# Optimization experiments

Measured on AMD Instinct MI355X. Metric: run time of the kernel, lower is better.

The kernel has to match this reference:

```python
import math
import jax, jax.numpy as jnp
import numpy as np

N_IMAGES = 32
TOTAL_Q = 2048
TOTAL_KV = 2048
Q_IN = 1024
KV_IN = Q_IN + 9
D_QK = 1024
D_V = 1024
N_HEADS = 16
TEMP = 1.0
SCALER = 1.0 / (TEMP * math.sqrt(D_QK // N_HEADS))


def _ragged_seg_ids(total, n_seg, seed):
    rng = np.random.default_rng(seed)
    lens = rng.multinomial(total - n_seg, np.ones(n_seg) / n_seg) + 1  # every segment nonempty
    return jnp.asarray(np.repeat(np.arange(n_seg), lens), dtype=jnp.int32)


def setup_inputs() -> dict:
    key = jax.random.key(0)
    ks = jax.random.split(key, 12)
    s = 0.02
    return {
        "A": jax.random.normal(ks[0], (TOTAL_Q, Q_IN), jnp.float32),
        "B0": jax.random.normal(ks[1], (TOTAL_KV, KV_IN), jnp.float32),
        "seg_q": _ragged_seg_ids(TOTAL_Q, N_IMAGES, 1),
        "seg_kv": _ragged_seg_ids(TOTAL_KV, N_IMAGES, 2),
        "Wq": jax.random.normal(ks[2], (Q_IN, D_QK), jnp.float32) * s,
        "bq": jax.random.normal(ks[3], (D_QK,), jnp.float32) * s,
        "Wk": jax.random.normal(ks[4], (KV_IN, D_QK), jnp.float32) * s,
        "bk": jax.random.normal(ks[5], (D_QK,), jnp.float32) * s,
        "Wv": jax.random.normal(ks[6], (KV_IN, D_V), jnp.float32) * s,
        "bv": jax.random.normal(ks[7], (D_V,), jnp.float32) * s,
        "Wf": jax.random.normal(ks[8], (D_V, Q_IN), jnp.float32) * s,
        "bf": jax.random.normal(ks[9], (Q_IN,), jnp.float32) * s,
    }


def reference(A, B0, seg_q, seg_kv, Wq, bq, Wk, bk, Wv, bv, Wf, bf):
    # Linear projections on packed rows
    q = (A @ Wq + bq).reshape(TOTAL_Q, N_HEADS, -1)     # [Nq, h, dqk]
    k = (B0 @ Wk + bk).reshape(TOTAL_KV, N_HEADS, -1)   # [Nk, h, dqk]
    v = (B0 @ Wv + bv).reshape(TOTAL_KV, N_HEADS, -1)   # [Nk, h, dv]
    # Per-segment attention expressed as a block mask (same math as the
    # original Python loop over splits)
    scores = jnp.einsum('ihd,khd->ihk', q, k) * SCALER  # [Nq, h, Nk]
    mask = (seg_q[:, None] == seg_kv[None, :])[:, None, :]  # [Nq, 1, Nk]
    neg = jnp.finfo(scores.dtype).min
    w = jax.nn.softmax(jnp.where(mask, scores, neg), axis=-1)
    wv = jnp.einsum('ihk,khd->ihd', w, v).reshape(TOTAL_Q, -1)  # [Nq, h*dv]
    return wv @ Wf + bf  # [Nq, q_in_dim]
```

## Files before the change

### kernel.cpp

```cpp
#include <hip/hip_runtime.h>
#include <hip/hip_bf16.h>
#include <math.h>

#define TOTAL_Q   2048
#define TOTAL_KV  2048
#define QIN       1024
#define KVIN      1033
#define KVIN_P    1056
#define DQK       1024
#define DV        1024
#define KVSTR     2048
#define SCALER    0.125f

typedef __bf16 bf16x8 __attribute__((ext_vector_type(8)));
typedef float  f32x4  __attribute__((ext_vector_type(4)));

__device__ __forceinline__ void glds16(const __hip_bfloat16* g, __bf16* l)
{
    __builtin_amdgcn_global_load_lds(
        (const __attribute__((address_space(1))) void*)g,
        (__attribute__((address_space(3))) void*)l,
        16, 0, 0);
}

__global__ __launch_bounds__(256)
void prep_k(const float* __restrict__ A,  const float* __restrict__ B0,
            const float* __restrict__ Wq, const float* __restrict__ Wk,
            const float* __restrict__ Wv, const float* __restrict__ Wf,
            const float* __restrict__ bf,
            __hip_bfloat16* __restrict__ Abf, __hip_bfloat16* __restrict__ B0bf,
            __hip_bfloat16* __restrict__ Wqt, __hip_bfloat16* __restrict__ Wkt,
            __hip_bfloat16* __restrict__ Wvt, __hip_bfloat16* __restrict__ Wft,
            float* __restrict__ outp)
{
    const int b   = blockIdx.x;
    const int tid = threadIdx.x;

    if (b < 2048) {
        int i = (b * 256 + tid) * 4;
        float4 f = *(const float4*)(A + i);
        __hip_bfloat16 o[4] = { __float2bfloat16(f.x), __float2bfloat16(f.y),
                                __float2bfloat16(f.z), __float2bfloat16(f.w) };
        *(uint2*)(Abf + i) = *(const uint2*)o;
        return;
    }
    if (b < 4160) {
        int idx = ((b - 2048) * 256 + tid) * 4;
        int r = idx / KVIN_P, c = idx - r * KVIN_P;
        __hip_bfloat16 o[4];
        #pragma unroll
        for (int j = 0; j < 4; ++j)
            o[j] = __float2bfloat16((c + j < KVIN) ? B0[(size_t)r * KVIN + c + j] : 0.f);
        *(uint2*)(B0bf + idx) = *(const uint2*)o;
        return;
    }
    if (b >= 8320) {
        int idx = ((b - 8320) * 256 + tid) * 4;
        int c = idx & 1023;
        float4 o = { bf[c], bf[c + 1], bf[c + 2], bf[c + 3] };
        *(float4*)(outp + idx) = o;
        return;
    }

    const float* W; __hip_bfloat16* Wt; int K, Kp, k0, n0;
    if (b < 6208) {
        int z = b - 4160;
        W  = (z >= 1024) ? Wf : Wq;
        Wt = (z >= 1024) ? Wft : Wqt;
        K = 1024; Kp = 1024;
        int rem = z & 1023;
        k0 = (rem & 31) * 32; n0 = (rem >> 5) * 32;
    } else {
        int z = b - 6208;
        W  = (z >= 1056) ? Wv : Wk;
        Wt = (z >= 1056) ? Wvt : Wkt;
        K = KVIN; Kp = KVIN_P;
        int rem = (z >= 1056) ? z - 1056 : z;
        k0 = (rem % 33) * 32; n0 = (rem / 33) * 32;
    }
    const int tx = tid & 31, ty = tid >> 5;
    __shared__ float tile[32][33];
    #pragma unroll
    for (int i = 0; i < 4; ++i) {
        int k = k0 + ty + i * 8;
        tile[ty + i * 8][tx] = (k < K) ? W[(size_t)k * 1024 + n0 + tx] : 0.f;
    }
    __syncthreads();
    #pragma unroll
    for (int i = 0; i < 4; ++i) {
        int n = n0 + ty + i * 8;
        Wt[(size_t)n * Kp + k0 + tx] = __float2bfloat16(tile[tx][ty + i * 8]);
    }
}

__device__ __forceinline__ int stage_cc(int lane)
{
    return (((lane & 3) ^ ((lane >> 3) & 3)) * 8);
}
__device__ __forceinline__ int frag_off(int row, int quad)
{
    return row * 32 + ((quad ^ ((row >> 1) & 3)) * 8);
}

__global__ __launch_bounds__(256)
void gemm_qkv(const __hip_bfloat16* __restrict__ Abf,
              const __hip_bfloat16* __restrict__ Wqt,
              const float* __restrict__ bq,
              __hip_bfloat16* __restrict__ qb,
              const __hip_bfloat16* __restrict__ B0bf,
              const __hip_bfloat16* __restrict__ Wkvt,
              const float* __restrict__ bk, const float* __restrict__ bv,
              __hip_bfloat16* __restrict__ kvb)
{
    __shared__ __bf16 As[2][128 * 32];
    __shared__ __bf16 Bs[2][64 * 32];

    int b = blockIdx.x;
    const __hip_bfloat16 *Ag, *Btg; const float *bias0, *bias1;
    __hip_bfloat16* C; int N, K, bx, by;
    if (b < 256) {
        Ag = Abf; Btg = Wqt; bias0 = bq; bias1 = bq; C = qb;
        N = 1024; K = 1024; bx = b & 15; by = b >> 4;
    } else {
        b -= 256;
        Ag = B0bf; Btg = Wkvt; bias0 = bk; bias1 = bv; C = kvb;
        N = 2048; K = KVIN_P; bx = b & 31; by = b >> 5;
    }
    const int row0 = by * 128, col0 = bx * 64;

    const int tid  = threadIdx.x;
    const int wave = tid >> 6, lane = tid & 63;
    const int quad = lane >> 4, l16 = lane & 15;
    const int wm = (wave >> 1) * 64, wn = (wave & 1) * 32;

    const int cr = lane >> 2;
    const int cc = stage_cc(lane);

    const __hip_bfloat16* gsrc[3];
    __bf16* ldst[2][3];
    #pragma unroll
    for (int i = 0; i < 3; ++i) {
        int c = wave * 3 + i;
        if (c < 8) {
            gsrc[i] = Ag  + (size_t)(row0 + c * 16 + cr) * K + cc;
            ldst[0][i] = &As[0][c * 512];
            ldst[1][i] = &As[1][c * 512];
        } else {
            gsrc[i] = Btg + (size_t)(col0 + (c - 8) * 16 + cr) * K + cc;
            ldst[0][i] = &Bs[0][(c - 8) * 512];
            ldst[1][i] = &Bs[1][(c - 8) * 512];
        }
    }

    f32x4 acc[4][2] = {};

    #pragma unroll
    for (int i = 0; i < 3; ++i)
        glds16(gsrc[i], ldst[0][i]);

    int cur = 0;
    for (int k0 = 0; k0 < K; k0 += 32) {
        __syncthreads();

        if (k0 + 32 < K) {
            #pragma unroll
            for (int i = 0; i < 3; ++i)
                glds16(gsrc[i] + k0 + 32, ldst[cur ^ 1][i]);
        }

        const __bf16* Ac = As[cur];
        const __bf16* Bc = Bs[cur];
        bf16x8 af[4], bfr[2];
        #pragma unroll
        for (int mi = 0; mi < 4; ++mi)
            af[mi] = *(const bf16x8*)&Ac[frag_off(wm + mi * 16 + l16, quad)];
        #pragma unroll
        for (int ni = 0; ni < 2; ++ni)
            bfr[ni] = *(const bf16x8*)&Bc[frag_off(wn + ni * 16 + l16, quad)];

        #pragma unroll
        for (int mi = 0; mi < 4; ++mi)
            #pragma unroll
            for (int ni = 0; ni < 2; ++ni)
                acc[mi][ni] = __builtin_amdgcn_mfma_f32_16x16x32_bf16(
                    af[mi], bfr[ni], acc[mi][ni], 0, 0, 0);
        cur ^= 1;
    }

    #pragma unroll
    for (int mi = 0; mi < 4; ++mi) {
        #pragma unroll
        for (int ni = 0; ni < 2; ++ni) {
            const int col = col0 + wn + ni * 16 + l16;
            const float bia = (col < 1024) ? bias0[col] : bias1[col - 1024];
            #pragma unroll
            for (int r = 0; r < 4; ++r) {
                const int row = row0 + wm + mi * 16 + quad * 4 + r;
                C[(size_t)row * N + col] = __float2bfloat16(acc[mi][ni][r] + bia);
            }
        }
    }
}

__global__ __launch_bounds__(256)
void gemm_out(const __hip_bfloat16* __restrict__ A,
              const __hip_bfloat16* __restrict__ Bt,
              float* __restrict__ C,
              int M, int N, int K)
{
    __shared__ __bf16 As[2][128 * 32];
    __shared__ __bf16 Bs[2][64 * 32];

    const int tid  = threadIdx.x;
    const int wave = tid >> 6, lane = tid & 63;
    const int quad = lane >> 4, l16 = lane & 15;
    const int wm = (wave >> 1) * 64;
    const int wn = (wave & 1) * 32;
    const int row0 = blockIdx.y * 128, col0 = blockIdx.x * 64;
    const int kz0 = blockIdx.z * (K / 2), kz1 = kz0 + K / 2;

    const int cr = lane >> 2;
    const int cc = stage_cc(lane);

    const __hip_bfloat16* gsrc[3];
    __bf16* ldst[2][3];
    #pragma unroll
    for (int i = 0; i < 3; ++i) {
        int c = wave * 3 + i;
        if (c < 8) {
            gsrc[i] = A  + (size_t)(row0 + c * 16 + cr) * K + cc;
            ldst[0][i] = &As[0][c * 512];
            ldst[1][i] = &As[1][c * 512];
        } else {
            gsrc[i] = Bt + (size_t)(col0 + (c - 8) * 16 + cr) * K + cc;
            ldst[0][i] = &Bs[0][(c - 8) * 512];
            ldst[1][i] = &Bs[1][(c - 8) * 512];
        }
    }

    f32x4 acc[4][2] = {};

    #pragma unroll
    for (int i = 0; i < 3; ++i)
        glds16(gsrc[i] + kz0, ldst[0][i]);

    int cur = 0;
    for (int k0 = kz0; k0 < kz1; k0 += 32) {
        __syncthreads();

        if (k0 + 32 < kz1) {
            #pragma unroll
            for (int i = 0; i < 3; ++i)
                glds16(gsrc[i] + k0 + 32, ldst[cur ^ 1][i]);
        }

        const __bf16* Ac = As[cur];
        const __bf16* Bc = Bs[cur];
        bf16x8 af[4], bfr[2];
        #pragma unroll
        for (int mi = 0; mi < 4; ++mi)
            af[mi] = *(const bf16x8*)&Ac[frag_off(wm + mi * 16 + l16, quad)];
        #pragma unroll
        for (int ni = 0; ni < 2; ++ni)
            bfr[ni] = *(const bf16x8*)&Bc[frag_off(wn + ni * 16 + l16, quad)];

        #pragma unroll
        for (int mi = 0; mi < 4; ++mi)
            #pragma unroll
            for (int ni = 0; ni < 2; ++ni)
                acc[mi][ni] = __builtin_amdgcn_mfma_f32_16x16x32_bf16(
                    af[mi], bfr[ni], acc[mi][ni], 0, 0, 0);
        cur ^= 1;
    }

    #pragma unroll
    for (int mi = 0; mi < 4; ++mi) {
        #pragma unroll
        for (int ni = 0; ni < 2; ++ni) {
            const int col = col0 + wn + ni * 16 + l16;
            #pragma unroll
            for (int r = 0; r < 4; ++r) {
                const int row = row0 + wm + mi * 16 + quad * 4 + r;
                atomicAdd(&C[(size_t)row * N + col], acc[mi][ni][r]);
            }
        }
    }
}

#define CH 64

__global__ __launch_bounds__(256)
void attn_mfma(const __hip_bfloat16* __restrict__ qg,
               const __hip_bfloat16* __restrict__ kg,
               const __hip_bfloat16* __restrict__ vg,
               const int* __restrict__ seg_q, const int* __restrict__ seg_kv,
               __hip_bfloat16* __restrict__ wv)
{
    const int h = blockIdx.x & 15;
    const int s = blockIdx.x >> 4;

    __shared__ int sb[4];
    __shared__ __bf16 Ks[CH][72];
    __shared__ __bf16 Vt[64][CH + 8];
    __shared__ __bf16 Ps[4][16][CH + 8];

    if (threadIdx.x == 0) {
        int lo, hi;
        lo = 0; hi = TOTAL_Q;
        while (lo < hi) { int m = (lo + hi) >> 1; if (seg_q[m] <  s) lo = m + 1; else hi = m; }
        sb[0] = lo;
        hi = TOTAL_Q;
        while (lo < hi) { int m = (lo + hi) >> 1; if (seg_q[m] <= s) lo = m + 1; else hi = m; }
        sb[1] = lo;
        lo = 0; hi = TOTAL_KV;
        while (lo < hi) { int m = (lo + hi) >> 1; if (seg_kv[m] <  s) lo = m + 1; else hi = m; }
        sb[2] = lo;
        hi = TOTAL_KV;
        while (lo < hi) { int m = (lo + hi) >> 1; if (seg_kv[m] <= s) lo = m + 1; else hi = m; }
        sb[3] = lo;
    }
    __syncthreads();
    const int qbeg = sb[0], qend = sb[1], kbeg = sb[2], kend = sb[3];

    const int tid  = threadIdx.x;
    const int wave = tid >> 6, lane = tid & 63;
    const int quad = lane >> 4, l16 = lane & 15;

    for (int qt = qbeg; qt < qend; qt += 64) {
        const int qrow = qt + wave * 16 + l16;
        const int qrc  = min(qrow, qend - 1);
        bf16x8 qf[2];
        qf[0] = *(const bf16x8*)(qg + (size_t)qrc * DQK + h * 64 + quad * 8);
        qf[1] = *(const bf16x8*)(qg + (size_t)qrc * DQK + h * 64 + 32 + quad * 8);

        float m[4]  = { -1e30f, -1e30f, -1e30f, -1e30f };
        float l[4]  = { 0.f, 0.f, 0.f, 0.f };
        f32x4 acc[4] = {};

        for (int c0 = kbeg; c0 < kend; c0 += CH) {
            const int cl = min(CH, kend - c0);
            __syncthreads();

            #pragma unroll
            for (int it = 0; it < 2; ++it) {
                int e = (it * 256 + tid) * 8;
                int r = e >> 6, d = e & 63;
                bf16x8 z = {};
                if (r < cl)
                    z = *(const bf16x8*)(kg + (size_t)(c0 + r) * KVSTR + h * 64 + d);
                *(bf16x8*)&Ks[r][d] = z;
            }
            #pragma unroll
            for (int it = 0; it < 4; ++it) {
                int e = (it * 256 + tid) * 4;
                int r = e >> 6, d = e & 63;
                __bf16 t0 = 0, t1 = 0, t2 = 0, t3 = 0;
                if (r < cl) {
                    bf16x8 vv;
                    uint2 uu = *(const uint2*)(vg + (size_t)(c0 + r) * KVSTR + h * 64 + d);
                    *(uint2*)&vv = uu;
                    t0 = vv[0]; t1 = vv[1]; t2 = vv[2]; t3 = vv[3];
                }
                Vt[d + 0][r] = t0; Vt[d + 1][r] = t1;
                Vt[d + 2][r] = t2; Vt[d + 3][r] = t3;
            }
            __syncthreads();

            f32x4 sc[4];
            #pragma unroll
            for (int t = 0; t < 4; ++t) {
                bf16x8 b0 = *(const bf16x8*)&Ks[t * 16 + l16][quad * 8];
                bf16x8 b1 = *(const bf16x8*)&Ks[t * 16 + l16][32 + quad * 8];
                f32x4 z = {};
                z = __builtin_amdgcn_mfma_f32_16x16x32_bf16(qf[0], b0, z, 0, 0, 0);
                z = __builtin_amdgcn_mfma_f32_16x16x32_bf16(qf[1], b1, z, 0, 0, 0);
                sc[t] = z;
            }

            float sv[4][4];
            #pragma unroll
            for (int t = 0; t < 4; ++t) {
                const bool ok = (c0 + t * 16 + l16) < kend;
                #pragma unroll
                for (int r = 0; r < 4; ++r)
                    sv[t][r] = ok ? sc[t][r] * SCALER : -1e30f;
            }

            #pragma unroll
            for (int r = 0; r < 4; ++r) {
                float mx = fmaxf(fmaxf(sv[0][r], sv[1][r]), fmaxf(sv[2][r], sv[3][r]));
                mx = fmaxf(mx, __shfl_xor(mx, 1));
                mx = fmaxf(mx, __shfl_xor(mx, 2));
                mx = fmaxf(mx, __shfl_xor(mx, 4));
                mx = fmaxf(mx, __shfl_xor(mx, 8));
                const float mn = fmaxf(m[r], mx);
                const float alpha = __expf(m[r] - mn);
                m[r] = mn;
                float rs = 0.f;
                #pragma unroll
                for (int t = 0; t < 4; ++t) {
                    const float p = __expf(sv[t][r] - mn);
                    sv[t][r] = p;
                    rs += p;
                }
                rs += __shfl_xor(rs, 1);
                rs += __shfl_xor(rs, 2);
                rs += __shfl_xor(rs, 4);
                rs += __shfl_xor(rs, 8);
                l[r] = l[r] * alpha + rs;
                #pragma unroll
                for (int dt = 0; dt < 4; ++dt) acc[dt][r] *= alpha;
            }

            #pragma unroll
            for (int t = 0; t < 4; ++t)
                #pragma unroll
                for (int r = 0; r < 4; ++r)
                    Ps[wave][quad * 4 + r][t * 16 + l16] = (__bf16)sv[t][r];
            __syncthreads();

            #pragma unroll
            for (int ks = 0; ks < 2; ++ks) {
                bf16x8 pa = *(const bf16x8*)&Ps[wave][l16][ks * 32 + quad * 8];
                #pragma unroll
                for (int dt = 0; dt < 4; ++dt) {
                    bf16x8 vbf = *(const bf16x8*)&Vt[dt * 16 + l16][ks * 32 + quad * 8];
                    acc[dt] = __builtin_amdgcn_mfma_f32_16x16x32_bf16(pa, vbf, acc[dt], 0, 0, 0);
                }
            }
        }

        float inv[4];
        #pragma unroll
        for (int r = 0; r < 4; ++r) inv[r] = 1.f / l[r];
        #pragma unroll
        for (int dt = 0; dt < 4; ++dt) {
            #pragma unroll
            for (int r = 0; r < 4; ++r) {
                const int row = qt + wave * 16 + quad * 4 + r;
                if (row < qend)
                    wv[(size_t)row * DV + h * 64 + dt * 16 + l16] =
                        __float2bfloat16(acc[dt][r] * inv[r]);
            }
        }
    }
}

extern "C" void kernel_launch(void* const* d_in, const int* in_sizes, int n_in,
                              void* d_out, int out_size, void* d_ws, size_t ws_size,
                              hipStream_t stream)
{
    const float* A     = (const float*)d_in[0];
    const float* B0    = (const float*)d_in[1];
    const int*   seg_q = (const int*)  d_in[2];
    const int*   seg_kv= (const int*)  d_in[3];
    const float* Wq    = (const float*)d_in[4];
    const float* bq    = (const float*)d_in[5];
    const float* Wk    = (const float*)d_in[6];
    const float* bk    = (const float*)d_in[7];
    const float* Wv    = (const float*)d_in[8];
    const float* bv    = (const float*)d_in[9];
    const float* Wf    = (const float*)d_in[10];
    const float* bf    = (const float*)d_in[11];
    float* out = (float*)d_out;

    __hip_bfloat16* B0bf = (__hip_bfloat16*)d_ws;
    __hip_bfloat16* Wqt  = B0bf + (size_t)TOTAL_KV * KVIN_P;
    __hip_bfloat16* Wkt  = Wqt  + (size_t)QIN * DQK;
    __hip_bfloat16* Wvt  = Wkt  + (size_t)DQK * KVIN_P;
    __hip_bfloat16* Wft  = Wvt  + (size_t)DV * KVIN_P;
    __hip_bfloat16* Abf  = Wft  + (size_t)DV * QIN;
    __hip_bfloat16* qb   = Abf  + (size_t)TOTAL_Q * QIN;
    __hip_bfloat16* kvb  = qb   + (size_t)TOTAL_Q * DQK;
    __hip_bfloat16* wvb  = Abf;

    const dim3 b256(256);

    prep_k<<<dim3(10368), b256, 0, stream>>>(A, B0, Wq, Wk, Wv, Wf, bf,
                                             Abf, B0bf, Wqt, Wkt, Wvt, Wft, out);

    gemm_qkv<<<dim3(768), b256, 0, stream>>>(Abf, Wqt, bq, qb,
                                             B0bf, Wkt, bk, bv, kvb);

    attn_mfma<<<dim3(32 * 16), b256, 0, stream>>>(qb, kvb, kvb + 1024, seg_q, seg_kv, wvb);

    gemm_out<<<dim3(QIN / 64, TOTAL_Q / 128, 2), b256, 0, stream>>>(
        wvb, Wft, out, TOTAL_Q, QIN, DV);
}
```

Before: 170.6 us.

## Fuse Q/K/V projections into the per-segment attention kernel

Removes the separate QKV GEMM launch. Each (segment, head) attention block now computes its own Q tile from A and Wq, and its K and V chunks from B0 and the concatenated Wk/Wv weights, directly into shared memory. This avoids writing q/k/v to global memory and reading them back, and drops one kernel launch. In exchange the projection GEMMs run with small 64-wide tiles, no double buffering and two barriers per k-step. K/V projections are also recomputed for every 64-row query tile, and padded chunks add wasted work, so total FLOPs grow.

Measured after the change: 227.2 us. +33.2%, slower.

```diff
diff --git a/kernel.cpp b/kernel.cpp
--- a/kernel.cpp
+++ b/kernel.cpp
@@ -9,7 +9,6 @@
 #define KVIN_P    1056
 #define DQK       1024
 #define DV        1024
-#define KVSTR     2048
 #define SCALER    0.125f
 
 typedef __bf16 bf16x8 __attribute__((ext_vector_type(8)));
@@ -21,6 +20,15 @@
         (const __attribute__((address_space(1))) void*)g,
         (__attribute__((address_space(3))) void*)l,
         16, 0, 0);
+}
+
+__device__ __forceinline__ int stage_cc(int lane)
+{
+    return (((lane & 3) ^ ((lane >> 3) & 3)) * 8);
+}
+__device__ __forceinline__ int frag_off(int row, int quad)
+{
+    return row * 32 + ((quad ^ ((row >> 1) & 3)) * 8);
 }
 
 __global__ __launch_bounds__(256)
@@ -93,216 +101,27 @@
     }
 }
 
-__device__ __forceinline__ int stage_cc(int lane)
-{
-    return (((lane & 3) ^ ((lane >> 3) & 3)) * 8);
-}
-__device__ __forceinline__ int frag_off(int row, int quad)
-{
-    return row * 32 + ((quad ^ ((row >> 1) & 3)) * 8);
-}
-
 __global__ __launch_bounds__(256)
-void gemm_qkv(const __hip_bfloat16* __restrict__ Abf,
-              const __hip_bfloat16* __restrict__ Wqt,
-              const float* __restrict__ bq,
-              __hip_bfloat16* __restrict__ qb,
-              const __hip_bfloat16* __restrict__ B0bf,
-              const __hip_bfloat16* __restrict__ Wkvt,
-              const float* __restrict__ bk, const float* __restrict__ bv,
-              __hip_bfloat16* __restrict__ kvb)
-{
-    __shared__ __bf16 As[2][128 * 32];
-    __shared__ __bf16 Bs[2][64 * 32];
-
-    int b = blockIdx.x;
-    const __hip_bfloat16 *Ag, *Btg; const float *bias0, *bias1;
-    __hip_bfloat16* C; int N, K, bx, by;
-    if (b < 256) {
-        Ag = Abf; Btg = Wqt; bias0 = bq; bias1 = bq; C = qb;
-        N = 1024; K = 1024; bx = b & 15; by = b >> 4;
-    } else {
-        b -= 256;
-        Ag = B0bf; Btg = Wkvt; bias0 = bk; bias1 = bv; C = kvb;
-        N = 2048; K = KVIN_P; bx = b & 31; by = b >> 5;
-    }
-    const int row0 = by * 128, col0 = bx * 64;
-
-    const int tid  = threadIdx.x;
-    const int wave = tid >> 6, lane = tid & 63;
-    const int quad = lane >> 4, l16 = lane & 15;
-    const int wm = (wave >> 1) * 64, wn = (wave & 1) * 32;
-
-    const int cr = lane >> 2;
-    const int cc = stage_cc(lane);
-
-    const __hip_bfloat16* gsrc[3];
-    __bf16* ldst[2][3];
-    #pragma unroll
-    for (int i = 0; i < 3; ++i) {
-        int c = wave * 3 + i;
-        if (c < 8) {
-            gsrc[i] = Ag  + (size_t)(row0 + c * 16 + cr) * K + cc;
-            ldst[0][i] = &As[0][c * 512];
-            ldst[1][i] = &As[1][c * 512];
-        } else {
-            gsrc[i] = Btg + (size_t)(col0 + (c - 8) * 16 + cr) * K + cc;
-            ldst[0][i] = &Bs[0][(c - 8) * 512];
-            ldst[1][i] = &Bs[1][(c - 8) * 512];
-        }
-    }
-
-    f32x4 acc[4][2] = {};
-
-    #pragma unroll
-    for (int i = 0; i < 3; ++i)
-        glds16(gsrc[i], ldst[0][i]);
-
-    int cur = 0;
-    for (int k0 = 0; k0 < K; k0 += 32) {
-        __syncthreads();
-
-        if (k0 + 32 < K) {
-            #pragma unroll
-            for (int i = 0; i < 3; ++i)
-                glds16(gsrc[i] + k0 + 32, ldst[cur ^ 1][i]);
-        }
-
-        const __bf16* Ac = As[cur];
-        const __bf16* Bc = Bs[cur];
-        bf16x8 af[4], bfr[2];
-        #pragma unroll
-        for (int mi = 0; mi < 4; ++mi)
-            af[mi] = *(const bf16x8*)&Ac[frag_off(wm + mi * 16 + l16, quad)];
-        #pragma unroll
-        for (int ni = 0; ni < 2; ++ni)
-            bfr[ni] = *(const bf16x8*)&Bc[frag_off(wn + ni * 16 + l16, quad)];
-
-        #pragma unroll
-        for (int mi = 0; mi < 4; ++mi)
-            #pragma unroll
-            for (int ni = 0; ni < 2; ++ni)
-                acc[mi][ni] = __builtin_amdgcn_mfma_f32_16x16x32_bf16(
-                    af[mi], bfr[ni], acc[mi][ni], 0, 0, 0);
-        cur ^= 1;
-    }
-
-    #pragma unroll
-    for (int mi = 0; mi < 4; ++mi) {
-        #pragma unroll
-        for (int ni = 0; ni < 2; ++ni) {
-            const int col = col0 + wn + ni * 16 + l16;
-            const float bia = (col < 1024) ? bias0[col] : bias1[col - 1024];
-            #pragma unroll
-            for (int r = 0; r < 4; ++r) {
-                const int row = row0 + wm + mi * 16 + quad * 4 + r;
-                C[(size_t)row * N + col] = __float2bfloat16(acc[mi][ni][r] + bia);
-            }
-        }
-    }
-}
-
-__global__ __launch_bounds__(256)
-void gemm_out(const __hip_bfloat16* __restrict__ A,
-              const __hip_bfloat16* __restrict__ Bt,
-              float* __restrict__ C,
-              int M, int N, int K)
-{
-    __shared__ __bf16 As[2][128 * 32];
-    __shared__ __bf16 Bs[2][64 * 32];
-
-    const int tid  = threadIdx.x;
-    const int wave = tid >> 6, lane = tid & 63;
-    const int quad = lane >> 4, l16 = lane & 15;
-    const int wm = (wave >> 1) * 64;
-    const int wn = (wave & 1) * 32;
-    const int row0 = blockIdx.y * 128, col0 = blockIdx.x * 64;
-    const int kz0 = blockIdx.z * (K / 2), kz1 = kz0 + K / 2;
-
-    const int cr = lane >> 2;
-    const int cc = stage_cc(lane);
-
-    const __hip_bfloat16* gsrc[3];
-    __bf16* ldst[2][3];
-    #pragma unroll
-    for (int i = 0; i < 3; ++i) {
-        int c = wave * 3 + i;
-        if (c < 8) {
-            gsrc[i] = A  + (size_t)(row0 + c * 16 + cr) * K + cc;
-            ldst[0][i] = &As[0][c * 512];
-            ldst[1][i] = &As[1][c * 512];
-        } else {
-            gsrc[i] = Bt + (size_t)(col0 + (c - 8) * 16 + cr) * K + cc;
-            ldst[0][i] = &Bs[0][(c - 8) * 512];
-            ldst[1][i] = &Bs[1][(c - 8) * 512];
-        }
-    }
-
-    f32x4 acc[4][2] = {};
-
-    #pragma unroll
-    for (int i = 0; i < 3; ++i)
-        glds16(gsrc[i] + kz0, ldst[0][i]);
-
-    int cur = 0;
-    for (int k0 = kz0; k0 < kz1; k0 += 32) {
-        __syncthreads();
-
-        if (k0 + 32 < kz1) {
-            #pragma unroll
-            for (int i = 0; i < 3; ++i)
-                glds16(gsrc[i] + k0 + 32, ldst[cur ^ 1][i]);
-        }
-
-        const __bf16* Ac = As[cur];
-        const __bf16* Bc = Bs[cur];
-        bf16x8 af[4], bfr[2];
-        #pragma unroll
-        for (int mi = 0; mi < 4; ++mi)
-            af[mi] = *(const bf16x8*)&Ac[frag_off(wm + mi * 16 + l16, quad)];
-        #pragma unroll
-        for (int ni = 0; ni < 2; ++ni)
-            bfr[ni] = *(const bf16x8*)&Bc[frag_off(wn + ni * 16 + l16, quad)];
-
-        #pragma unroll
-        for (int mi = 0; mi < 4; ++mi)
-            #pragma unroll
-            for (int ni = 0; ni < 2; ++ni)
-                acc[mi][ni] = __builtin_amdgcn_mfma_f32_16x16x32_bf16(
-                    af[mi], bfr[ni], acc[mi][ni], 0, 0, 0);
-        cur ^= 1;
-    }
-
-    #pragma unroll
-    for (int mi = 0; mi < 4; ++mi) {
-        #pragma unroll
-        for (int ni = 0; ni < 2; ++ni) {
-            const int col = col0 + wn + ni * 16 + l16;
-            #pragma unroll
-            for (int r = 0; r < 4; ++r) {
-                const int row = row0 + wm + mi * 16 + quad * 4 + r;
-                atomicAdd(&C[(size_t)row * N + col], acc[mi][ni][r]);
-            }
-        }
-    }
-}
-
-#define CH 64
-
-__global__ __launch_bounds__(256)
-void attn_mfma(const __hip_bfloat16* __restrict__ qg,
-               const __hip_bfloat16* __restrict__ kg,
-               const __hip_bfloat16* __restrict__ vg,
-               const int* __restrict__ seg_q, const int* __restrict__ seg_kv,
-               __hip_bfloat16* __restrict__ wv)
+void attn_fused(const __hip_bfloat16* __restrict__ Abf,
+                const __hip_bfloat16* __restrict__ B0bf,
+                const __hip_bfloat16* __restrict__ Wqt,
+                const __hip_bfloat16* __restrict__ Wkvt,
+                const float* __restrict__ bq, const float* __restrict__ bk,
+                const float* __restrict__ bv,
+                const int* __restrict__ seg_q, const int* __restrict__ seg_kv,
+                __hip_bfloat16* __restrict__ wv)
 {
     const int h = blockIdx.x & 15;
     const int s = blockIdx.x >> 4;
 
     __shared__ int sb[4];
-    __shared__ __bf16 Ks[CH][72];
-    __shared__ __bf16 Vt[64][CH + 8];
-    __shared__ __bf16 Ps[4][16][CH + 8];
+    __shared__ __bf16 qS[64][72];
+    __shared__ __bf16 Ks[64][72];
+    __shared__ __bf16 Vt[64][72];
+    __shared__ __bf16 Ps[4][16][72];
+    __shared__ __bf16 As[64 * 32];
+    __shared__ __bf16 Bs[64 * 32];
+    __shared__ __bf16 Bs2[64 * 32];
 
     if (threadIdx.x == 0) {
         int lo, hi;
@@ -326,45 +145,128 @@
     const int wave = tid >> 6, lane = tid & 63;
     const int quad = lane >> 4, l16 = lane & 15;
 
+    const int cr = lane >> 2;
+    const int cc = stage_cc(lane);
+
+    float bqv[4], bkv[4], bvv[4];
+    #pragma unroll
+    for (int nt = 0; nt < 4; ++nt) {
+        bqv[nt] = bq[h * 64 + nt * 16 + l16];
+        bkv[nt] = bk[h * 64 + nt * 16 + l16];
+        bvv[nt] = bv[h * 64 + nt * 16 + l16];
+    }
+
+    const __hip_bfloat16* kv_wsrc[3];
+    __bf16* kv_dst[3];
+    int kv_achunk[3];
+    #pragma unroll
+    for (int i = 0; i < 3; ++i) {
+        int c = wave * 3 + i;
+        if (c < 4) {
+            kv_achunk[i] = c;
+            kv_wsrc[i] = nullptr;
+            kv_dst[i] = &As[c * 512];
+        } else if (c < 8) {
+            kv_achunk[i] = -1;
+            kv_wsrc[i] = Wkvt + (size_t)(h * 64 + (c - 4) * 16 + cr) * KVIN_P + cc;
+            kv_dst[i] = &Bs[(c - 4) * 512];
+        } else {
+            kv_achunk[i] = -1;
+            kv_wsrc[i] = Wkvt + (size_t)(1024 + h * 64 + (c - 8) * 16 + cr) * KVIN_P + cc;
+            kv_dst[i] = &Bs2[(c - 8) * 512];
+        }
+    }
+
     for (int qt = qbeg; qt < qend; qt += 64) {
-        const int qrow = qt + wave * 16 + l16;
-        const int qrc  = min(qrow, qend - 1);
+        {
+            const __hip_bfloat16* gsrc[2];
+            __bf16* ldst[2];
+            #pragma unroll
+            for (int i = 0; i < 2; ++i) {
+                int c = wave * 2 + i;
+                if (c < 4) {
+                    int g = min(qt + c * 16 + cr, qend - 1);
+                    gsrc[i] = Abf + (size_t)g * QIN + cc;
+                    ldst[i] = &As[c * 512];
+                } else {
+                    gsrc[i] = Wqt + (size_t)(h * 64 + (c - 4) * 16 + cr) * DQK + cc;
+                    ldst[i] = &Bs[(c - 4) * 512];
+                }
+            }
+
+            f32x4 accq[4] = {};
+            for (int k0 = 0; k0 < 1024; k0 += 32) {
+                glds16(gsrc[0] + k0, ldst[0]);
+                glds16(gsrc[1] + k0, ldst[1]);
+                __syncthreads();
+                bf16x8 af = *(const bf16x8*)&As[frag_off(wave * 16 + l16, quad)];
+                bf16x8 bfr[4];
+                #pragma unroll
+                for (int nt = 0; nt < 4; ++nt)
+                    bfr[nt] = *(const bf16x8*)&Bs[frag_off(nt * 16 + l16, quad)];
+                #pragma unroll
+                for (int nt = 0; nt < 4; ++nt)
+                    accq[nt] = __builtin_amdgcn_mfma_f32_16x16x32_bf16(af, bfr[nt], accq[nt], 0, 0, 0);
+                __syncthreads();
+            }
+            #pragma unroll
+            for (int nt = 0; nt < 4; ++nt)
+                #pragma unroll
+                for (int r = 0; r < 4; ++r)
+                    qS[wave * 16 + quad * 4 + r][nt * 16 + l16] =
+                        (__bf16)(accq[nt][r] + bqv[nt]);
+        }
         bf16x8 qf[2];
-        qf[0] = *(const bf16x8*)(qg + (size_t)qrc * DQK + h * 64 + quad * 8);
-        qf[1] = *(const bf16x8*)(qg + (size_t)qrc * DQK + h * 64 + 32 + quad * 8);
+        qf[0] = *(const bf16x8*)&qS[wave * 16 + l16][quad * 8];
+        qf[1] = *(const bf16x8*)&qS[wave * 16 + l16][32 + quad * 8];
 
         float m[4]  = { -1e30f, -1e30f, -1e30f, -1e30f };
         float l[4]  = { 0.f, 0.f, 0.f, 0.f };
         f32x4 acc[4] = {};
 
-        for (int c0 = kbeg; c0 < kend; c0 += CH) {
-            const int cl = min(CH, kend - c0);
-            __syncthreads();
-
-            #pragma unroll
-            for (int it = 0; it < 2; ++it) {
-                int e = (it * 256 + tid) * 8;
-                int r = e >> 6, d = e & 63;
-                bf16x8 z = {};
-                if (r < cl)
-                    z = *(const bf16x8*)(kg + (size_t)(c0 + r) * KVSTR + h * 64 + d);
-                *(bf16x8*)&Ks[r][d] = z;
-            }
-            #pragma unroll
-            for (int it = 0; it < 4; ++it) {
-                int e = (it * 256 + tid) * 4;
-                int r = e >> 6, d = e & 63;
-                __bf16 t0 = 0, t1 = 0, t2 = 0, t3 = 0;
-                if (r < cl) {
-                    bf16x8 vv;
-                    uint2 uu = *(const uint2*)(vg + (size_t)(c0 + r) * KVSTR + h * 64 + d);
-                    *(uint2*)&vv = uu;
-                    t0 = vv[0]; t1 = vv[1]; t2 = vv[2]; t3 = vv[3];
+        for (int c0 = kbeg; c0 < kend; c0 += 64) {
+            {
+                const __hip_bfloat16* gsrc[3];
+                #pragma unroll
+                for (int i = 0; i < 3; ++i) {
+                    if (kv_achunk[i] >= 0) {
+                        int g = min(c0 + kv_achunk[i] * 16 + cr, TOTAL_KV - 1);
+                        gsrc[i] = B0bf + (size_t)g * KVIN_P + cc;
+                    } else {
+                        gsrc[i] = kv_wsrc[i];
+                    }
                 }
-                Vt[d + 0][r] = t0; Vt[d + 1][r] = t1;
-                Vt[d + 2][r] = t2; Vt[d + 3][r] = t3;
-            }
-            __syncthreads();
+
+                f32x4 acck[4] = {}, accv[4] = {};
+                for (int k0 = 0; k0 < KVIN_P; k0 += 32) {
+                    #pragma unroll
+                    for (int i = 0; i < 3; ++i)
+                        glds16(gsrc[i] + k0, kv_dst[i]);
+                    __syncthreads();
+                    bf16x8 af = *(const bf16x8*)&As[frag_off(wave * 16 + l16, quad)];
+                    bf16x8 bk8[4], bv8[4];
+                    #pragma unroll
+                    for (int nt = 0; nt < 4; ++nt) {
+                        bk8[nt] = *(const bf16x8*)&Bs [frag_off(nt * 16 + l16, quad)];
+                        bv8[nt] = *(const bf16x8*)&Bs2[frag_off(nt * 16 + l16, quad)];
+                    }
+                    #pragma unroll
+                    for (int nt = 0; nt < 4; ++nt) {
+                        acck[nt] = __builtin_amdgcn_mfma_f32_16x16x32_bf16(af, bk8[nt], acck[nt], 0, 0, 0);
+                        accv[nt] = __builtin_amdgcn_mfma_f32_16x16x32_bf16(af, bv8[nt], accv[nt], 0, 0, 0);
+                    }
+                    __syncthreads();
+                }
+                #pragma unroll
+                for (int nt = 0; nt < 4; ++nt)
+                    #pragma unroll
+                    for (int r = 0; r < 4; ++r) {
+                        const int row = wave * 16 + quad * 4 + r;
+                        Ks[row][nt * 16 + l16] = (__bf16)(acck[nt][r] + bkv[nt]);
+                        Vt[nt * 16 + l16][row] = (__bf16)(accv[nt][r] + bvv[nt]);
+                    }
+                __syncthreads();
+            }
 
             f32x4 sc[4];
             #pragma unroll
@@ -441,6 +343,92 @@
                 if (row < qend)
                     wv[(size_t)row * DV + h * 64 + dt * 16 + l16] =
                         __float2bfloat16(acc[dt][r] * inv[r]);
+            }
+        }
+        __syncthreads();
+    }
+}
+
+__global__ __launch_bounds__(256)
+void gemm_out(const __hip_bfloat16* __restrict__ A,
+              const __hip_bfloat16* __restrict__ Bt,
+              float* __restrict__ C,
+              int M, int N, int K)
+{
+    __shared__ __bf16 As[2][128 * 32];
+    __shared__ __bf16 Bs[2][64 * 32];
+
+    const int tid  = threadIdx.x;
+    const int wave = tid >> 6, lane = tid & 63;
+    const int quad = lane >> 4, l16 = lane & 15;
+    const int wm = (wave >> 1) * 64;
+    const int wn = (wave & 1) * 32;
+    const int row0 = blockIdx.y * 128, col0 = blockIdx.x * 64;
+    const int kz0 = blockIdx.z * (K / 2), kz1 = kz0 + K / 2;
+
+    const int cr = lane >> 2;
+    const int cc = stage_cc(lane);
+
+    const __hip_bfloat16* gsrc[3];
+    __bf16* ldst[2][3];
+    #pragma unroll
+    for (int i = 0; i < 3; ++i) {
+        int c = wave * 3 + i;
+        if (c < 8) {
+            gsrc[i] = A  + (size_t)(row0 + c * 16 + cr) * K + cc;
+            ldst[0][i] = &As[0][c * 512];
+            ldst[1][i] = &As[1][c * 512];
+        } else {
+            gsrc[i] = Bt + (size_t)(col0 + (c - 8) * 16 + cr) * K + cc;
+            ldst[0][i] = &Bs[0][(c - 8) * 512];
+            ldst[1][i] = &Bs[1][(c - 8) * 512];
+        }
+    }
+
+    f32x4 acc[4][2] = {};
+
+    #pragma unroll
+    for (int i = 0; i < 3; ++i)
+        glds16(gsrc[i] + kz0, ldst[0][i]);
+
+    int cur = 0;
+    for (int k0 = kz0; k0 < kz1; k0 += 32) {
+        __syncthreads();
+
+        if (k0 + 32 < kz1) {
+            #pragma unroll
+            for (int i = 0; i < 3; ++i)
+                glds16(gsrc[i] + k0 + 32, ldst[cur ^ 1][i]);
+        }
+
+        const __bf16* Ac = As[cur];
+        const __bf16* Bc = Bs[cur];
+        bf16x8 af[4], bfr[2];
+        #pragma unroll
+        for (int mi = 0; mi < 4; ++mi)
+            af[mi] = *(const bf16x8*)&Ac[frag_off(wm + mi * 16 + l16, quad)];
+        #pragma unroll
+        for (int ni = 0; ni < 2; ++ni)
+            bfr[ni] = *(const bf16x8*)&Bc[frag_off(wn + ni * 16 + l16, quad)];
+
+        #pragma unroll
+        for (int mi = 0; mi < 4; ++mi)
+            #pragma unroll
+            for (int ni = 0; ni < 2; ++ni)
+                acc[mi][ni] = __builtin_amdgcn_mfma_f32_16x16x32_bf16(
+                    af[mi], bfr[ni], acc[mi][ni], 0, 0, 0);
+        cur ^= 1;
+    }
+
+    #pragma unroll
+    for (int mi = 0; mi < 4; ++mi) {
+        #pragma unroll
+        for (int ni = 0; ni < 2; ++ni) {
+            const int col = col0 + wn + ni * 16 + l16;
+            #pragma unroll
+            for (int r = 0; r < 4; ++r) {
+                const int row = row0 + wm + mi * 16 + quad * 4 + r;
+                atomicAdd(&C[(size_t)row * N + col], acc[mi][ni][r]);
             }
         }
     }
@@ -470,19 +458,15 @@
     __hip_bfloat16* Wvt  = Wkt  + (size_t)DQK * KVIN_P;
     __hip_bfloat16* Wft  = Wvt  + (size_t)DV * KVIN_P;
     __hip_bfloat16* Abf  = Wft  + (size_t)DV * QIN;
-    __hip_bfloat16* qb   = Abf  + (size_t)TOTAL_Q * QIN;
-    __hip_bfloat16* kvb  = qb   + (size_t)TOTAL_Q * DQK;
-    __hip_bfloat16* wvb  = Abf;
+    __hip_bfloat16* wvb  = Abf  + (size_t)TOTAL_Q * QIN;
 
     const dim3 b256(256);
 
     prep_k<<<dim3(10368), b256, 0, stream>>>(A, B0, Wq, Wk, Wv, Wf, bf,
                                              Abf, B0bf, Wqt, Wkt, Wvt, Wft, out);
 
-    gemm_qkv<<<dim3(768), b256, 0, stream>>>(Abf, Wqt, bq, qb,
-                                             B0bf, Wkt, bk, bv, kvb);
-
-    attn_mfma<<<dim3(32 * 16), b256, 0, stream>>>(qb, kvb, kvb + 1024, seg_q, seg_kv, wvb);
+    attn_fused<<<dim3(32 * 16), b256, 0, stream>>>(Abf, B0bf, Wqt, Wkt,
+                                                   bq, bk, bv, seg_q, seg_kv, wvb);
 
     gemm_out<<<dim3(QIN / 64, TOTAL_Q / 128, 2), b256, 0, stream>>>(
         wvb, Wft, out, TOTAL_Q, QIN, DV);
```
